# Performance work log

Hardware: AMD Instinct MI355X
Metric: run time of the kernel (lower is better)

The kernel has to match this reference:

```python
import jax, jax.numpy as jnp
import numpy as np

N_E = 8192
E_DIM = 64
BETA = 0.25
N_TOKENS = 32768


def setup_inputs() -> dict:
    key = jax.random.key(0)
    k1, k2 = jax.random.split(key)
    x = jax.random.normal(k1, (N_TOKENS, E_DIM), dtype=jnp.float32)
    # nn.Embedding weight initialized uniform(-1/n_e, 1/n_e)
    codebook = jax.random.uniform(k2, (N_E, E_DIM), dtype=jnp.float32,
                                  minval=-1.0 / N_E, maxval=1.0 / N_E)
    return {"x": x, "codebook": codebook, "start": 0, "end": N_E, "use_sk": 0}


def reference(x, codebook, start, end, use_sk):
    # use_sk=0 -> argmin branch (sinkhorn branch calls external helper, not exercised)
    latent = x.reshape(-1, E_DIM)                       # [N, D]
    cb = codebook[start:end]                            # [K, D]
    # squared euclidean distances: ||z||^2 + ||e||^2 - 2 z.e
    d = (jnp.sum(latent * latent, axis=1, keepdims=True)
         + jnp.sum(cb * cb, axis=1)[None, :]
         - 2.0 * jnp.einsum('nd,kd->nk', latent, cb))   # [N, K]
    indices = jnp.argmin(d, axis=-1) + start            # [N]
    x_q = codebook[indices].reshape(x.shape)            # gather
    sg = jax.lax.stop_gradient
    commitment_loss = jnp.mean((sg(x_q) - x) ** 2)
    codebook_loss = jnp.mean((x_q - sg(x)) ** 2)
    loss = codebook_loss + BETA * commitment_loss
    x_q_st = x + sg(x_q - x)                            # straight-through estimator
    indices = indices.reshape(x.shape[:-1])
    return x_q_st, loss, indices
```

## Files before the change

### kernel.cpp

```cpp
#include <hip/hip_runtime.h>
#include <math.h>


#define N_E    8192
#define EDIM   64
#define NTOK   32768
#define NELEM  (NTOK * EDIM)
#define CSZ    32
#define WINDOW 3e-4f
#define TTOK   256
#define TCODE  1024
#define SROW   72
#define TOKB   16
#define CCAP   64
#define KCAP   320

typedef __attribute__((ext_vector_type(8)))  short          short8;
typedef __attribute__((ext_vector_type(8)))  unsigned short ushort8v;
typedef __attribute__((ext_vector_type(16))) float          f32x16;

__device__ __forceinline__ unsigned short f2bf(float f) {
  unsigned int u = __float_as_uint(f);
  return (unsigned short)((u + 0x7FFFu + ((u >> 16) & 1u)) >> 16);
}
__device__ __forceinline__ unsigned short f2h(float f) {
  union { _Float16 h; unsigned short u; } cv; cv.h = (_Float16)f; return cv.u;
}
__device__ __forceinline__ float h2f(unsigned short b) {
  union { _Float16 h; unsigned short u; } cv; cv.u = b; return (float)cv.h;
}
__device__ __forceinline__ float max16(const f32x16 a) {
  float m = fmaxf(fmaxf(a[0], a[1]), a[2]);
  m = fmaxf(fmaxf(m, a[3]),  a[4]);
  m = fmaxf(fmaxf(m, a[5]),  a[6]);
  m = fmaxf(fmaxf(m, a[7]),  a[8]);
  m = fmaxf(fmaxf(m, a[9]),  a[10]);
  m = fmaxf(fmaxf(m, a[11]), a[12]);
  m = fmaxf(fmaxf(m, a[13]), a[14]);
  return fmaxf(m, a[15]);
}
__device__ __forceinline__ float sx_of(const float4* xl4) {
#pragma clang fp contract(off)
  float a0=0,a1=0,a2=0,a3=0,a4=0,a5=0,a6=0,a7=0;
#pragma unroll
  for (int i = 0; i < 8; ++i) {
    float4 pA = xl4[2*i], pB = xl4[2*i+1];
    a0 += pA.x * pA.x; a1 += pA.y * pA.y; a2 += pA.z * pA.z; a3 += pA.w * pA.w;
    a4 += pB.x * pB.x; a5 += pB.y * pB.y; a6 += pB.z * pB.z; a7 += pB.w * pB.w;
  }
  return ((a0+a1) + (a2+a3)) + ((a4+a5) + (a6+a7));
}

__global__ __launch_bounds__(256) void vq_sc(const float* __restrict__ cb,
                                             float* __restrict__ sc,
                                             unsigned short* __restrict__ cbf) {
#pragma clang fp contract(off)
  int r = blockIdx.x * 256 + threadIdx.x;
  const float4* c4 = (const float4*)(cb + (size_t)r * EDIM);
  float sval = sx_of(c4);
  sc[r] = sval;
  unsigned short* dst = cbf + (size_t)r * EDIM;
#pragma unroll
  for (int h = 0; h < 8; ++h) {
    float4 fA = c4[2*h], fB = c4[2*h+1];
    ushort8v o = {f2bf(fA.x), f2bf(fA.y), f2bf(fA.z), f2bf(fA.w),
                  f2bf(fB.x), f2bf(fB.y), f2bf(fB.z), f2bf(fB.w)};
    *(ushort8v*)&dst[h * 8] = o;
  }
}

__global__ __launch_bounds__(256, 3) void vq_pass1(
    const float* __restrict__ x, const unsigned short* __restrict__ cbf,
    unsigned int* __restrict__ cand,
    const int* __restrict__ p_start, const int* __restrict__ p_end) {
  __shared__ unsigned short Cs[128 * SROW];
  int tid = threadIdx.x;
  int tb = blockIdx.x;
  int cbk = blockIdx.y;
  int s = *p_start, e = *p_end;

  int lane = tid & 63, wv = tid >> 6;
  int half = lane >> 5, ln = lane & 31;
  int tokbase = wv * 64;

  const ushort8v* cg0 = (const ushort8v*)(cbf + (size_t)cbk * TCODE * EDIM);
#pragma unroll
  for (int p = 0; p < 4; ++p) {
    int idx = tid + p * 256;
    int row = idx >> 3, h = idx & 7;
    *(ushort8v*)&Cs[row * SROW + h * 8] = cg0[idx];
  }

  short8 bfr[2][4];
#pragma unroll
  for (int tg = 0; tg < 2; ++tg) {
    const float* xrow =
        x + (size_t)(tb * TTOK + tokbase + tg * 32 + ln) * EDIM + half * 8;
#pragma unroll
    for (int ks = 0; ks < 4; ++ks) {
      float4 fA = *(const float4*)(xrow + ks * 16);
      float4 fB = *(const float4*)(xrow + ks * 16 + 4);
      short8 v = {(short)f2bf(fA.x), (short)f2bf(fA.y), (short)f2bf(fA.z),
                  (short)f2bf(fA.w), (short)f2bf(fB.x), (short)f2bf(fB.y),
                  (short)f2bf(fB.z), (short)f2bf(fB.w)};
      bfr[tg][ks] = v;
    }
  }
  __syncthreads();

  unsigned s0=~0u,s1=~0u,s2=~0u,s3=~0u,s4=~0u,s5=~0u,s6=~0u,s7=~0u,s8=~0u;
  unsigned m0=0,m1=0,m2=0,m3=0,m4=0,m5=0,m6=0,m7=0,m8=0;
  unsigned bmap = 0u;
  float lm0 = INFINITY, lm1 = INFINITY;

  for (int nb = 0; nb < 8; ++nb) {
    ushort8v creg[4];
    if (nb < 7) {
      const ushort8v* cg =
          (const ushort8v*)(cbf + ((size_t)cbk * TCODE + (nb + 1) * 128) * EDIM);
#pragma unroll
      for (int p = 0; p < 4; ++p) creg[p] = cg[tid + p * 256];
    }
#pragma unroll
    for (int cp = 0; cp < 2; ++cp) {
      f32x16 acc[2][2];
#pragma unroll
      for (int tg = 0; tg < 2; ++tg)
#pragma unroll
        for (int c2 = 0; c2 < 2; ++c2) acc[tg][c2] = (f32x16)0.0f;
#pragma unroll
      for (int ks = 0; ks < 4; ++ks)
#pragma unroll
        for (int c2 = 0; c2 < 2; ++c2) {
          int ct = cp * 2 + c2;
          short8 a = *(const short8*)&Cs[(ct*32 + ln) * SROW + ks*16 + half*8];
          acc[0][c2] = __builtin_amdgcn_mfma_f32_32x32x16_bf16(a, bfr[0][ks],
                                                               acc[0][c2], 0, 0, 0);
          acc[1][c2] = __builtin_amdgcn_mfma_f32_32x32x16_bf16(a, bfr[1][ks],
                                                               acc[1][c2], 0, 0, 0);
        }
#pragma unroll
      for (int c2 = 0; c2 < 2; ++c2) {
        int cidL = nb * 4 + cp * 2 + c2;
        int c0 = cbk * TCODE + cidL * 32;
        bool full = (c0 >= s) && (c0 + 32 <= e);
        float v0, v1;
        if (full) {
          v0 = max16(acc[0][c2]);
          v1 = max16(acc[1][c2]);
        } else {
          v0 = -INFINITY; v1 = -INFINITY;
#pragma unroll
          for (int r = 0; r < 16; ++r) {
            int code = c0 + (r & 3) + 8 * (r >> 2) + 4 * half;
            if (code >= s && code < e) {
              v0 = fmaxf(v0, acc[0][c2][r]);
              v1 = fmaxf(v1, acc[1][c2][r]);
            }
          }
        }
        v0 = fmaxf(v0, __shfl_xor(v0, 32, 64));
        v1 = fmaxf(v1, __shfl_xor(v1, 32, 64));
        unsigned short hh0 = f2h(-2.0f * v0);
        unsigned short hh1 = f2h(-2.0f * v1);
        float mv0 = h2f(hh0), mv1 = h2f(hh1);
        lm0 = fminf(lm0, mv0);
        lm1 = fminf(lm1, mv1);
        bool a0 = (mv0 <= lm0 + WINDOW);
        bool a1 = (mv1 <= lm1 + WINDOW);
        unsigned b0 = 0, b1 = 0;
        if (a0 | a1) {
          float t0 = v0 - WINDOW * 0.5f;
          float t1 = v1 - WINDOW * 0.5f;
#pragma unroll
          for (int r = 0; r < 16; ++r) {
            int pos = (r & 3) + 8 * (r >> 2) + 4 * half;
            if (acc[0][c2][r] >= t0) b0 |= (1u << pos);
            if (acc[1][c2][r] >= t1) b1 |= (1u << pos);
          }
          b0 |= __shfl_xor(b0, 32, 64);
          b1 |= __shfl_xor(b1, 32, 64);
        }
        bool aown = half ? a1 : a0;
        if (aown) {
          bmap |= 1u << cidL;
          unsigned short hh = half ? hh1 : hh0;
          unsigned bs = half ? b1 : b0;
          unsigned mono = (unsigned)hh ^ ((hh & 0x8000u) ? 0xFFFFu : 0x8000u);
          unsigned p = (mono << 16) | (unsigned)cidL;
          unsigned pm = bs;
          if (p < s8) {
#define INS2_(SK, SM) { bool lt_ = p < (SK); unsigned tk_ = (SK), tm_ = (SM); \
            if (lt_) { (SK) = p; (SM) = pm; p = tk_; pm = tm_; } }
            INS2_(s0,m0) INS2_(s1,m1) INS2_(s2,m2) INS2_(s3,m3) INS2_(s4,m4)
            INS2_(s5,m5) INS2_(s6,m6) INS2_(s7,m7) INS2_(s8,m8)
#undef INS2_
          }
        }
      }
    }
    __syncthreads();
    if (nb < 7) {
#pragma unroll
      for (int p = 0; p < 4; ++p) {
        int idx = tid + p * 256;
        int row = idx >> 3, h = idx & 7;
        *(ushort8v*)&Cs[row * SROW + h * 8] = creg[p];
      }
    }
    __syncthreads();
  }

  {
    float lminf = half ? lm1 : lm0;
    float thr = lminf + WINDOW;
    unsigned rec[8], msk[8];
#define EMIT_(J, S, M) { unsigned mono_ = (S) >> 16; \
    unsigned hh_ = (mono_ & 0x8000u) ? (mono_ ^ 0x8000u) : (mono_ ^ 0xFFFFu); \
    float v_ = h2f((unsigned short)hh_); \
    rec[J] = (v_ <= thr) ? ((hh_ << 16) | ((S) & 0xFFFFu)) : 0xFFFFFFFFu; \
    msk[J] = (M); }
    EMIT_(0, s0, m0) EMIT_(1, s1, m1) EMIT_(2, s2, m2) EMIT_(3, s3, m3)
    EMIT_(4, s4, m4) EMIT_(5, s5, m5) EMIT_(6, s6, m6) EMIT_(7, s7, m7)
#undef EMIT_
    {
      unsigned mono_ = s8 >> 16;
      unsigned hh_ = (mono_ & 0x8000u) ? (mono_ ^ 0x8000u) : (mono_ ^ 0xFFFFu);
      float v8 = h2f((unsigned short)hh_);
      if (v8 <= thr) rec[7] = 0x0000FFFEu;
    }
    int token = tb * TTOK + tokbase + lane;
#pragma unroll
    for (int j = 0; j < 8; ++j) {
      cand[(size_t)(cbk * 8 + j) * NTOK + token] = rec[j];
      cand[(size_t)(64 + cbk * 8 + j) * NTOK + token] = msk[j];
    }
    cand[(size_t)(128 + cbk) * NTOK + token] = bmap;
  }
}

__global__ __launch_bounds__(256) void vq_rescue(
    const float* __restrict__ x, const float* __restrict__ cb,
    const float* __restrict__ sc, const unsigned int* __restrict__ cand,
    float* __restrict__ out_xq, float* __restrict__ out_idx,
    float* __restrict__ partial,
    const int* __restrict__ p_start, const int* __restrict__ p_end) {
#pragma clang fp contract(off)
  __shared__ float xsh[TOKB][64];
  __shared__ float sxs[TOKB];
  __shared__ unsigned short lst[TOKB][CCAP];
  __shared__ unsigned short clst[TOKB][KCAP];
  __shared__ int ccnt[TOKB], kcnt[TOKB];
  int tid  = threadIdx.x;
  int wv   = tid >> 6;
  int lane = tid & 63;
  int blk  = blockIdx.x;
  int s = *p_start, e = *p_end;

  if (tid < TOKB) { ccnt[tid] = 0; kcnt[tid] = 0; }
#pragma unroll
  for (int p = 0; p < (TOKB * CCAP) / 256; ++p)
    ((unsigned short*)lst)[tid + p * 256] = 0xFFFFu;
  __syncthreads();

  if (tid < 128) {
    int tl = tid >> 3, q = tid & 7;
    int gtok = blk * TOKB + tl;
    unsigned rv[8], mk[8];
#pragma unroll
    for (int j = 0; j < 8; ++j) {
      rv[j] = cand[(size_t)(q * 8 + j) * NTOK + gtok];
      mk[j] = cand[(size_t)(64 + q * 8 + j) * NTOK + gtok];
    }
    float m = INFINITY;
#pragma unroll
    for (int j = 0; j < 8; ++j) {
      unsigned cid = rv[j] & 0xFFFFu;
      float v = (cid < 32u) ? h2f((unsigned short)(rv[j] >> 16)) : INFINITY;
      m = fminf(m, v);
    }
    m = fminf(m, __shfl_xor(m, 1, 64));
    m = fminf(m, __shfl_xor(m, 2, 64));
    m = fminf(m, __shfl_xor(m, 4, 64));
    float thr = m + WINDOW;
    bool marker = ((rv[7] & 0xFFFFu) == 0xFFFEu);
    if (!marker) {
#pragma unroll
      for (int j = 0; j < 8; ++j) {
        unsigned cid = rv[j] & 0xFFFFu;
        if (cid < 32u && h2f((unsigned short)(rv[j] >> 16)) <= thr) {
          unsigned bits = mk[j];
          int n = __popc(bits);
          int base = atomicAdd(&ccnt[tl], n);
          if (base + n <= CCAP) {
            int kb = (q * 32 + (int)cid) * CSZ;
            while (bits) {
              int bpos = __ffs(bits) - 1; bits &= bits - 1;
              lst[tl][base++] = (unsigned short)(kb + bpos);
            }
          } else {
            int kb2 = atomicAdd(&kcnt[tl], 1);
            if (kb2 < KCAP) clst[tl][kb2] = (unsigned short)(q * 32 + (int)cid);
          }
        }
      }
    } else {
      unsigned cid0 = rv[0] & 0xFFFFu;
      float v0 = (cid0 < 32u) ? h2f((unsigned short)(rv[0] >> 16)) : INFINITY;
      if (v0 <= thr) {
        unsigned b0 = cand[(size_t)(128 + q) * NTOK + gtok];
        int n = __popc(b0);
        int base = atomicAdd(&kcnt[tl], n);
        while (b0) { int j = __ffs(b0) - 1; b0 &= b0 - 1;
          if (base < KCAP) clst[tl][base] = (unsigned short)(q * 32 + j); ++base; }
      }
    }
  } else if (tid < 192) {
    int t = tid - 128;
#pragma unroll
    for (int p = 0; p < 4; ++p) {
      int idx = t + p * 64;
      int tl = idx >> 4, seg = idx & 15;
      *(float4*)&xsh[tl][seg * 4] =
          ((const float4*)(x + (size_t)(blk * TOKB + tl) * EDIM))[seg];
    }
  } else if (tid < 192 + TOKB) {
    int tl = tid - 192;
    sxs[tl] = sx_of((const float4*)(x + (size_t)(blk * TOKB + tl) * EDIM));
  }
  __syncthreads();

#define EVAL_CODE_BODY(K_, XL4) do {                                           \
    const float4* c4_ = (const float4*)(cb + (size_t)(K_) * EDIM);             \
    float t0_=0.0f,t1_=0.0f,t2_=0.0f,t3_=0.0f;                                 \
    _Pragma("unroll")                                                          \
    for (int i_ = 0; i_ < 8; ++i_) {                 \
      float4 v_ = c4_[2*i_ + h5_];                                             \
      float4 p_ = (XL4)[2*i_ + h5_];                                           \
      t0_ += v_.x * p_.x; t1_ += v_.y * p_.y;                                  \
      t2_ += v_.z * p_.z; t3_ += v_.w * p_.w;                                  \
    }                                                                          \
    s2_ = (t0_ + t1_) + (t2_ + t3_);              \
  } while (0)

#define FINISH_CODE(K_, ACT, SX, BP) do {                                      \
    float tt_ = s2_ + __shfl_xor(s2_, 1, 64);                                  \
    if ((ACT) && (K_) >= s && (K_) < e) {                                      \
      float d_ = ((SX) + sc[K_]) - 2.0f * tt_;                                 \
      unsigned db_ = __float_as_uint(d_);                                      \
      unsigned en_ = db_ ^ ((unsigned)((int)db_ >> 31) | 0x80000000u);         \
      unsigned long long pk_ = ((unsigned long long)en_ << 32) | (unsigned)(K_);\
      if (pk_ < (BP)) (BP) = pk_;                                              \
    }                                                                          \
  } while (0)

  float sg[4];
#pragma unroll
  for (int ti = 0; ti < 4; ++ti) {
    int tl = wv * 4 + ti;
    int gtok = blk * TOKB + tl;
    const float4* xl4 = (const float4*)xsh[tl];
    float sx = sxs[tl];
    unsigned long long bp = ~0ull;
    int ci_ = lane >> 1, h5_ = lane & 1;
    int nc = ccnt[tl]; if (nc > CCAP) nc = CCAP;
    for (int b0 = 0; b0 < nc; b0 += 32) {
      int nb = nc - b0; if (nb > 32) nb = 32;
      int kraw = (ci_ < nb) ? (int)lst[tl][b0 + ci_] : 0xFFFF;
      bool act = (kraw != 0xFFFF);
      int k_ = act ? kraw : 0;
      float s2_ = 0.0f;
      if (act) EVAL_CODE_BODY(k_, xl4);
      FINISH_CODE(k_, act, sx, bp);
    }
    int nk = kcnt[tl]; if (nk > KCAP) nk = KCAP;
    for (int i = 0; i < nk; ++i) {
      int k_ = (int)clst[tl][i] * CSZ + ci_;
      float s2_;
      EVAL_CODE_BODY(k_, xl4);
      FINISH_CODE(k_, true, sx, bp);
    }
#pragma unroll
    for (int off = 32; off >= 1; off >>= 1) {
      unsigned long long o = __shfl_xor(bp, off, 64);
      if (o < bp) bp = o;
    }
    int bidx = (int)(unsigned)(bp & 0xFFFFFFFFull) & (N_E - 1);

    float xx = xsh[tl][lane];
    float qv = cb[(size_t)bidx * EDIM + lane];
    float diff = qv - xx;
    out_xq[(size_t)gtok * EDIM + lane] = xx + diff;
    if (lane == 0) out_idx[gtok] = (float)bidx;
    float l = diff * diff;
#pragma unroll
    for (int off = 32; off >= 1; off >>= 1) l += __shfl_down(l, off, 64);
    sg[ti] = l;
  }
#undef EVAL_CODE_BODY
#undef FINISH_CODE
  if (lane == 0)
    partial[blk * 4 + wv] = (sg[0] + sg[1]) + (sg[2] + sg[3]);
}

__global__ __launch_bounds__(256) void vq_loss(const float* __restrict__ partial,
                                               float* __restrict__ out_loss) {
  int tid = threadIdx.x;
  float s = 0.0f;
  for (int i = tid; i < NTOK / 4; i += 256) s += partial[i];
#pragma unroll
  for (int off = 32; off >= 1; off >>= 1) s += __shfl_down(s, off, 64);
  __shared__ float sdata[4];
  if ((tid & 63) == 0) sdata[tid >> 6] = s;
  __syncthreads();
  if (tid == 0) {
    float total = (sdata[0] + sdata[1]) + (sdata[2] + sdata[3]);
    float m = total * (1.0f / (float)NELEM);
    out_loss[0] = m + 0.25f * m;
  }
}

extern "C" void kernel_launch(void* const* d_in, const int* in_sizes, int n_in,
                              void* d_out, int out_size, void* d_ws, size_t ws_size,
                              hipStream_t stream) {
  const float* x  = (const float*)d_in[0];
  const float* cb = (const float*)d_in[1];
  const int* p_start = (const int*)d_in[2];
  const int* p_end   = (const int*)d_in[3];

  float* ws = (float*)d_ws;
  float* sc      = ws;
  float* partial = ws + N_E;
  unsigned short* cbf  = (unsigned short*)(ws + 2 * N_E);
  unsigned int*   cand = (unsigned int*)(cbf + (size_t)N_E * EDIM);

  float* out      = (float*)d_out;
  float* out_xq   = out;
  float* out_loss = out + NELEM;
  float* out_idx  = out + NELEM + 1;

  vq_sc<<<N_E / 256, 256, 0, stream>>>(cb, sc, cbf);
  dim3 g1(NTOK / TTOK, N_E / TCODE);
  vq_pass1<<<g1, 256, 0, stream>>>(x, cbf, cand, p_start, p_end);
  vq_rescue<<<NTOK / TOKB, 256, 0, stream>>>(x, cb, sc, cand, out_xq, out_idx,
                                             partial, p_start, p_end);
  vq_loss<<<1, 256, 0, stream>>>(partial, out_loss);
}
```

Baseline: 179.0 us.

## Pre-convert x to bf16, double-buffer codebook LDS, and repack candidate records token-major

Several changes land together. x is converted to bf16 once in a merged prep kernel, so each of the eight pass1 codebook-chunk blocks no longer re-reads and re-converts fp32 x. The codebook shared-memory tile is double-buffered, which removes one barrier per iteration, and the first MFMA of each tile uses a zero accumulator instead of explicit zeroing. Candidate records are written token-major as contiguous uint4s with a separate bitmap array, so the rescue kernel reads them with coalesced vector loads, and the overflow marker handling changes (skipping slots already expanded). The cost is doubled LDS, which may lower occupancy, plus an extra bf16 x buffer in the workspace.

After: 189.1 us. 1.06x slower.

```diff
diff --git a/kernel.cpp b/kernel.cpp
--- a/kernel.cpp
+++ b/kernel.cpp
@@ -51,29 +51,45 @@
   return ((a0+a1) + (a2+a3)) + ((a4+a5) + (a6+a7));
 }
 
-__global__ __launch_bounds__(256) void vq_sc(const float* __restrict__ cb,
-                                             float* __restrict__ sc,
-                                             unsigned short* __restrict__ cbf) {
+__global__ __launch_bounds__(256) void vq_prep(const float* __restrict__ cb,
+                                               const float* __restrict__ x,
+                                               float* __restrict__ sc,
+                                               unsigned short* __restrict__ cbf,
+                                               unsigned short* __restrict__ xbf) {
 #pragma clang fp contract(off)
-  int r = blockIdx.x * 256 + threadIdx.x;
-  const float4* c4 = (const float4*)(cb + (size_t)r * EDIM);
-  float sval = sx_of(c4);
-  sc[r] = sval;
-  unsigned short* dst = cbf + (size_t)r * EDIM;
-#pragma unroll
-  for (int h = 0; h < 8; ++h) {
-    float4 fA = c4[2*h], fB = c4[2*h+1];
-    ushort8v o = {f2bf(fA.x), f2bf(fA.y), f2bf(fA.z), f2bf(fA.w),
-                  f2bf(fB.x), f2bf(fB.y), f2bf(fB.z), f2bf(fB.w)};
-    *(ushort8v*)&dst[h * 8] = o;
+  int bid = blockIdx.x;
+  if (bid < N_E / 256) {
+    int r = bid * 256 + threadIdx.x;
+    const float4* c4 = (const float4*)(cb + (size_t)r * EDIM);
+    float sval = sx_of(c4);
+    sc[r] = sval;
+    unsigned short* dst = cbf + (size_t)r * EDIM;
+#pragma unroll
+    for (int h = 0; h < 8; ++h) {
+      float4 fA = c4[2*h], fB = c4[2*h+1];
+      ushort8v o = {f2bf(fA.x), f2bf(fA.y), f2bf(fA.z), f2bf(fA.w),
+                    f2bf(fB.x), f2bf(fB.y), f2bf(fB.z), f2bf(fB.w)};
+      *(ushort8v*)&dst[h * 8] = o;
+    }
+  } else {
+    int r = (bid - N_E / 256) * 256 + threadIdx.x;
+    const float4* c4 = (const float4*)(x + (size_t)r * EDIM);
+    unsigned short* dst = xbf + (size_t)r * EDIM;
+#pragma unroll
+    for (int h = 0; h < 8; ++h) {
+      float4 fA = c4[2*h], fB = c4[2*h+1];
+      ushort8v o = {f2bf(fA.x), f2bf(fA.y), f2bf(fA.z), f2bf(fA.w),
+                    f2bf(fB.x), f2bf(fB.y), f2bf(fB.z), f2bf(fB.w)};
+      *(ushort8v*)&dst[h * 8] = o;
+    }
   }
 }
 
 __global__ __launch_bounds__(256, 3) void vq_pass1(
-    const float* __restrict__ x, const unsigned short* __restrict__ cbf,
-    unsigned int* __restrict__ cand,
+    const unsigned short* __restrict__ xbf, const unsigned short* __restrict__ cbf,
+    unsigned int* __restrict__ cand, unsigned int* __restrict__ bmapb,
     const int* __restrict__ p_start, const int* __restrict__ p_end) {
-  __shared__ unsigned short Cs[128 * SROW];
+  __shared__ unsigned short Cs[2][128 * SROW];
   int tid = threadIdx.x;
   int tb = blockIdx.x;
   int cbk = blockIdx.y;
@@ -88,23 +104,17 @@
   for (int p = 0; p < 4; ++p) {
     int idx = tid + p * 256;
     int row = idx >> 3, h = idx & 7;
-    *(ushort8v*)&Cs[row * SROW + h * 8] = cg0[idx];
+    *(ushort8v*)&Cs[0][row * SROW + h * 8] = cg0[idx];
   }
 
   short8 bfr[2][4];
 #pragma unroll
   for (int tg = 0; tg < 2; ++tg) {
-    const float* xrow =
-        x + (size_t)(tb * TTOK + tokbase + tg * 32 + ln) * EDIM + half * 8;
-#pragma unroll
-    for (int ks = 0; ks < 4; ++ks) {
-      float4 fA = *(const float4*)(xrow + ks * 16);
-      float4 fB = *(const float4*)(xrow + ks * 16 + 4);
-      short8 v = {(short)f2bf(fA.x), (short)f2bf(fA.y), (short)f2bf(fA.z),
-                  (short)f2bf(fA.w), (short)f2bf(fB.x), (short)f2bf(fB.y),
-                  (short)f2bf(fB.z), (short)f2bf(fB.w)};
-      bfr[tg][ks] = v;
-    }
+    const unsigned short* xrow =
+        xbf + (size_t)(tb * TTOK + tokbase + tg * 32 + ln) * EDIM + half * 8;
+#pragma unroll
+    for (int ks = 0; ks < 4; ++ks)
+      bfr[tg][ks] = *(const short8*)&xrow[ks * 16];
   }
   __syncthreads();
 
@@ -112,6 +122,7 @@
   unsigned m0=0,m1=0,m2=0,m3=0,m4=0,m5=0,m6=0,m7=0,m8=0;
   unsigned bmap = 0u;
   float lm0 = INFINITY, lm1 = INFINITY;
+  const f32x16 zro = (f32x16)0.0f;
 
   for (int nb = 0; nb < 8; ++nb) {
     ushort8v creg[4];
@@ -121,19 +132,23 @@
 #pragma unroll
       for (int p = 0; p < 4; ++p) creg[p] = cg[tid + p * 256];
     }
+    int cur = nb & 1;
 #pragma unroll
     for (int cp = 0; cp < 2; ++cp) {
       f32x16 acc[2][2];
 #pragma unroll
-      for (int tg = 0; tg < 2; ++tg)
-#pragma unroll
-        for (int c2 = 0; c2 < 2; ++c2) acc[tg][c2] = (f32x16)0.0f;
-#pragma unroll
-      for (int ks = 0; ks < 4; ++ks)
+      for (int c2 = 0; c2 < 2; ++c2) {
+        int ct = cp * 2 + c2;
+        short8 a = *(const short8*)&Cs[cur][(ct*32 + ln) * SROW + half*8];
+        acc[0][c2] = __builtin_amdgcn_mfma_f32_32x32x16_bf16(a, bfr[0][0], zro, 0, 0, 0);
+        acc[1][c2] = __builtin_amdgcn_mfma_f32_32x32x16_bf16(a, bfr[1][0], zro, 0, 0, 0);
+      }
+#pragma unroll
+      for (int ks = 1; ks < 4; ++ks)
 #pragma unroll
         for (int c2 = 0; c2 < 2; ++c2) {
           int ct = cp * 2 + c2;
-          short8 a = *(const short8*)&Cs[(ct*32 + ln) * SROW + ks*16 + half*8];
+          short8 a = *(const short8*)&Cs[cur][(ct*32 + ln) * SROW + ks*16 + half*8];
           acc[0][c2] = __builtin_amdgcn_mfma_f32_32x32x16_bf16(a, bfr[0][ks],
                                                                acc[0][c2], 0, 0, 0);
           acc[1][c2] = __builtin_amdgcn_mfma_f32_32x32x16_bf16(a, bfr[1][ks],
@@ -199,13 +214,12 @@
         }
       }
     }
-    __syncthreads();
     if (nb < 7) {
 #pragma unroll
       for (int p = 0; p < 4; ++p) {
         int idx = tid + p * 256;
         int row = idx >> 3, h = idx & 7;
-        *(ushort8v*)&Cs[row * SROW + h * 8] = creg[p];
+        *(ushort8v*)&Cs[cur ^ 1][row * SROW + h * 8] = creg[p];
       }
     }
     __syncthreads();
@@ -227,21 +241,23 @@
       unsigned mono_ = s8 >> 16;
       unsigned hh_ = (mono_ & 0x8000u) ? (mono_ ^ 0x8000u) : (mono_ ^ 0xFFFFu);
       float v8 = h2f((unsigned short)hh_);
-      if (v8 <= thr) rec[7] = 0x0000FFFEu;
+      if (v8 <= thr) rec[7] |= 0x8000u;
     }
     int token = tb * TTOK + tokbase + lane;
-#pragma unroll
-    for (int j = 0; j < 8; ++j) {
-      cand[(size_t)(cbk * 8 + j) * NTOK + token] = rec[j];
-      cand[(size_t)(64 + cbk * 8 + j) * NTOK + token] = msk[j];
-    }
-    cand[(size_t)(128 + cbk) * NTOK + token] = bmap;
+    uint4* dst = (uint4*)(cand + ((size_t)token * 8 + cbk) * 16);
+    uint4 o0; o0.x = rec[0]; o0.y = rec[1]; o0.z = rec[2]; o0.w = rec[3];
+    uint4 o1; o1.x = rec[4]; o1.y = rec[5]; o1.z = rec[6]; o1.w = rec[7];
+    uint4 o2; o2.x = msk[0]; o2.y = msk[1]; o2.z = msk[2]; o2.w = msk[3];
+    uint4 o3; o3.x = msk[4]; o3.y = msk[5]; o3.z = msk[6]; o3.w = msk[7];
+    dst[0] = o0; dst[1] = o1; dst[2] = o2; dst[3] = o3;
+    bmapb[(size_t)token * 8 + cbk] = bmap;
   }
 }
 
 __global__ __launch_bounds__(256) void vq_rescue(
     const float* __restrict__ x, const float* __restrict__ cb,
     const float* __restrict__ sc, const unsigned int* __restrict__ cand,
+    const unsigned int* __restrict__ bmapb,
     float* __restrict__ out_xq, float* __restrict__ out_idx,
     float* __restrict__ partial,
     const int* __restrict__ p_start, const int* __restrict__ p_end) {
@@ -266,29 +282,26 @@
   if (tid < 128) {
     int tl = tid >> 3, q = tid & 7;
     int gtok = blk * TOKB + tl;
-    unsigned rv[8], mk[8];
-#pragma unroll
-    for (int j = 0; j < 8; ++j) {
-      rv[j] = cand[(size_t)(q * 8 + j) * NTOK + gtok];
-      mk[j] = cand[(size_t)(64 + q * 8 + j) * NTOK + gtok];
-    }
+    const uint4* rp = (const uint4*)(cand + ((size_t)gtok * 8 + q) * 16);
+    uint4 A0 = rp[0], A1 = rp[1], M0 = rp[2], M1 = rp[3];
+    unsigned rv[8] = {A0.x, A0.y, A0.z, A0.w, A1.x, A1.y, A1.z, A1.w};
+    unsigned mk[8] = {M0.x, M0.y, M0.z, M0.w, M1.x, M1.y, M1.z, M1.w};
     float m = INFINITY;
 #pragma unroll
-    for (int j = 0; j < 8; ++j) {
-      unsigned cid = rv[j] & 0xFFFFu;
-      float v = (cid < 32u) ? h2f((unsigned short)(rv[j] >> 16)) : INFINITY;
-      m = fminf(m, v);
-    }
+    for (int j = 0; j < 8; ++j)
+      m = fminf(m, h2f((unsigned short)(rv[j] >> 16)));
     m = fminf(m, __shfl_xor(m, 1, 64));
     m = fminf(m, __shfl_xor(m, 2, 64));
     m = fminf(m, __shfl_xor(m, 4, 64));
     float thr = m + WINDOW;
-    bool marker = ((rv[7] & 0xFFFFu) == 0xFFFEu);
-    if (!marker) {
-#pragma unroll
-      for (int j = 0; j < 8; ++j) {
-        unsigned cid = rv[j] & 0xFFFFu;
-        if (cid < 32u && h2f((unsigned short)(rv[j] >> 16)) <= thr) {
+    bool marker = (rv[7] != 0xFFFFFFFFu) && ((rv[7] & 0x8000u) != 0u);
+    unsigned slotbits = 0u;
+#pragma unroll
+    for (int j = 0; j < 8; ++j) {
+      if (rv[j] != 0xFFFFFFFFu) {
+        unsigned cid = rv[j] & 0x1Fu;
+        slotbits |= 1u << cid;
+        if (h2f((unsigned short)(rv[j] >> 16)) <= thr) {
           unsigned bits = mk[j];
           int n = __popc(bits);
           int base = atomicAdd(&ccnt[tl], n);
@@ -304,15 +317,15 @@
           }
         }
       }
-    } else {
-      unsigned cid0 = rv[0] & 0xFFFFu;
-      float v0 = (cid0 < 32u) ? h2f((unsigned short)(rv[0] >> 16)) : INFINITY;
-      if (v0 <= thr) {
-        unsigned b0 = cand[(size_t)(128 + q) * NTOK + gtok];
-        int n = __popc(b0);
-        int base = atomicAdd(&kcnt[tl], n);
-        while (b0) { int j = __ffs(b0) - 1; b0 &= b0 - 1;
-          if (base < KCAP) clst[tl][base] = (unsigned short)(q * 32 + j); ++base; }
+    }
+    if (marker) {
+      unsigned bm = bmapb[(size_t)gtok * 8 + q] & ~slotbits;
+      int n = __popc(bm);
+      int base = atomicAdd(&kcnt[tl], n);
+      while (bm) {
+        int j = __ffs(bm) - 1; bm &= bm - 1;
+        if (base < KCAP) clst[tl][base] = (unsigned short)(q * 32 + j);
+        ++base;
       }
     }
   } else if (tid < 192) {
@@ -432,17 +445,19 @@
   float* sc      = ws;
   float* partial = ws + N_E;
   unsigned short* cbf  = (unsigned short*)(ws + 2 * N_E);
-  unsigned int*   cand = (unsigned int*)(cbf + (size_t)N_E * EDIM);
+  unsigned short* xbf  = cbf + (size_t)N_E * EDIM;
+  unsigned int*   cand = (unsigned int*)(xbf + (size_t)NTOK * EDIM);
+  unsigned int*   bmapb = cand + (size_t)NTOK * 8 * 16;
 
   float* out      = (float*)d_out;
   float* out_xq   = out;
   float* out_loss = out + NELEM;
   float* out_idx  = out + NELEM + 1;
 
-  vq_sc<<<N_E / 256, 256, 0, stream>>>(cb, sc, cbf);
+  vq_prep<<<(N_E + NTOK) / 256, 256, 0, stream>>>(cb, x, sc, cbf, xbf);
   dim3 g1(NTOK / TTOK, N_E / TCODE);
-  vq_pass1<<<g1, 256, 0, stream>>>(x, cbf, cand, p_start, p_end);
-  vq_rescue<<<NTOK / TOKB, 256, 0, stream>>>(x, cb, sc, cand, out_xq, out_idx,
+  vq_pass1<<<g1, 256, 0, stream>>>(xbf, cbf, cand, bmapb, p_start, p_end);
+  vq_rescue<<<NTOK / TOKB, 256, 0, stream>>>(x, cb, sc, cand, bmapb, out_xq, out_idx,
                                              partial, p_start, p_end);
   vq_loss<<<1, 256, 0, stream>>>(partial, out_loss);
 }
```
